# Kernel tuning notes

Measured on AMD Instinct MI355X. Metric: run time of the kernel, lower is better.

## Reference

```python
import jax, jax.numpy as jnp
import numpy as np

EMBED_DIM = 64
HIDDEN_DIM = 320
CONTEXT_DIM = 768

def setup_inputs() -> dict:
    key = jax.random.key(0)
    k1, k2, k3, k4, k5 = jax.random.split(key, 5)
    B, T, S = 4, 4096, 4096
    tokens = jax.random.normal(k1, (B, T, HIDDEN_DIM), dtype=jnp.float32)
    context = jax.random.normal(k2, (B, S, CONTEXT_DIM), dtype=jnp.float32)
    # nn.Linear(in, out, bias=False) weights, stored as [out, in] like torch
    sq = 1.0 / np.sqrt(HIDDEN_DIM)
    sk = 1.0 / np.sqrt(CONTEXT_DIM)
    Wq = jax.random.uniform(k3, (EMBED_DIM, HIDDEN_DIM), minval=-sq, maxval=sq, dtype=jnp.float32)
    Wk = jax.random.uniform(k4, (EMBED_DIM, CONTEXT_DIM), minval=-sk, maxval=sk, dtype=jnp.float32)
    Wv = jax.random.uniform(k5, (HIDDEN_DIM, CONTEXT_DIM), minval=-sk, maxval=sk, dtype=jnp.float32)
    return {"tokens": tokens, "context": context, "Wq": Wq, "Wk": Wk, "Wv": Wv}

def reference(tokens, context, Wq, Wk, Wv):
    # Q: [B,T,E], K: [B,S,E], V: [B,S,Hd]
    Q = jnp.einsum('bth,eh->bte', tokens, Wq)
    K = jnp.einsum('bsc,ec->bse', context, Wk)
    V = jnp.einsum('bsc,hc->bsh', context, Wv)
    scores = jnp.einsum('bte,bse->bts', Q, K) / np.sqrt(EMBED_DIM)
    attn = jax.nn.softmax(scores, axis=-1)  # [B,T,S] full score matrix as in original
    ctx_vecs = jnp.einsum('bts,bsh->bth', attn, V)
    return ctx_vecs
```

## Files before the change

kernel.cpp:

```cpp
#include <hip/hip_runtime.h>
#include <hip/hip_bf16.h>

typedef _Float16 half4_t  __attribute__((ext_vector_type(4)));
typedef _Float16 half8_t  __attribute__((ext_vector_type(8)));
typedef float    float4_t __attribute__((ext_vector_type(4)));

#define MFMA16x32(a, b, c) __builtin_amdgcn_mfma_f32_16x16x32_f16(a, b, c, 0, 0, 0)

template <int KTOT, int NT, int MODE>
__device__ __forceinline__ void proj_body(const float* __restrict__ A,
                                          const float* __restrict__ W,
                                          _Float16* __restrict__ out, float sc,
                                          int m0, int n0, int htg0,
                                          _Float16* Ach, _Float16* Bch) {
  constexpr int NCH = KTOT / 64;
  constexpr int NTIL = NT / 16;
  const int tid = threadIdx.x, w = tid >> 6, lane = tid & 63;
  const int G = lane >> 4, l15 = lane & 15;

  float4_t acc[NTIL];
#pragma unroll
  for (int nt = 0; nt < NTIL; ++nt) acc[nt] = {0.f, 0.f, 0.f, 0.f};

  float4_t areg[4], wreg[NTIL];
  auto ldA = [&](int kc) {
#pragma unroll
    for (int t = 0; t < 4; ++t) {
      int idx = t * 256 + tid;
      areg[t] = *(const float4_t*)(A + (size_t)(m0 + (idx >> 4)) * KTOT + kc * 64 + (idx & 15) * 4);
    }
  };
  auto ldW = [&](int kc) {
#pragma unroll
    for (int t = 0; t < NTIL; ++t) {
      int idx = t * 256 + tid;
      wreg[t] = *(const float4_t*)(W + (size_t)(n0 + (idx >> 4)) * KTOT + kc * 64 + (idx & 15) * 4);
    }
  };

  ldA(0); ldW(0);
  for (int kc = 0; kc < NCH; ++kc) {
    __syncthreads();
#pragma unroll
    for (int t = 0; t < 4; ++t) {
      int idx = t * 256 + tid;
      half4_t h = {(_Float16)areg[t][0], (_Float16)areg[t][1], (_Float16)areg[t][2], (_Float16)areg[t][3]};
      *(half4_t*)(Ach + (idx >> 4) * 72 + (idx & 15) * 4) = h;
    }
#pragma unroll
    for (int t = 0; t < NTIL; ++t) {
      int idx = t * 256 + tid;
      half4_t h = {(_Float16)wreg[t][0], (_Float16)wreg[t][1], (_Float16)wreg[t][2], (_Float16)wreg[t][3]};
      *(half4_t*)(Bch + (idx >> 4) * 72 + (idx & 15) * 4) = h;
    }
    __syncthreads();
    if (kc + 1 < NCH) { ldA(kc + 1); ldW(kc + 1); }
#pragma unroll
    for (int c = 0; c < 2; ++c) {
      half8_t af = *(const half8_t*)(Ach + (w * 16 + l15) * 72 + c * 32 + 8 * G);
#pragma unroll
      for (int nt = 0; nt < NTIL; ++nt) {
        half8_t bf = *(const half8_t*)(Bch + (nt * 16 + l15) * 72 + c * 32 + 8 * G);
        acc[nt] = MFMA16x32(af, bf, acc[nt]);
      }
    }
  }

  if constexpr (MODE <= 1) {
#pragma unroll
    for (int nt = 0; nt < NTIL; ++nt)
#pragma unroll
      for (int r = 0; r < 4; ++r)
        out[(size_t)(m0 + w * 16 + 4 * G + r) * 64 + nt * 16 + l15] = (_Float16)(acc[nt][r] * sc);
  } else {
    __syncthreads();
#pragma unroll
    for (int nt = 0; nt < NTIL; ++nt) {
      half4_t h = {(_Float16)acc[nt][0], (_Float16)acc[nt][1], (_Float16)acc[nt][2], (_Float16)acc[nt][3]};
      *(half4_t*)(Bch + (nt * 16 + l15) * 72 + w * 16 + 4 * G) = h;
    }
    __syncthreads();
#pragma unroll
    for (int rep = 0; rep < 5; ++rep) {
      int idx = w * 5 + rep;
      int c2 = idx / 10, htl = idx % 10;
      half8_t fr = *(const half8_t*)(Bch + (htl * 16 + l15) * 72 + c2 * 32 + 8 * G);
      int sg = m0 + c2 * 32;
      int b = sg >> 12, c2b = (sg & 4095) >> 5;
      int htg = htg0 + htl;
      *(half8_t*)(out + ((size_t)((b * 128 + c2b) * 20 + htg)) * 512 + lane * 8) = fr;
    }
  }
}

__global__ __launch_bounds__(256, 2)
void qkv_proj_kernel(const float* __restrict__ tokens, const float* __restrict__ context,
                     const float* __restrict__ Wq, const float* __restrict__ Wk,
                     const float* __restrict__ Wv, _Float16* __restrict__ Q,
                     _Float16* __restrict__ K, _Float16* __restrict__ V) {
  __shared__ alignas(16) _Float16 smem[16128];
  _Float16* Ach = smem;
  _Float16* Bch = smem + 64 * 72;
  const int bx = blockIdx.x;
  const float qsc = 0.125f * 1.44269504088896f;
  if (bx < 512) {
    int y = bx >> 8, mb = bx & 255;
    proj_body<768, 160, 2>(context, Wv, V, 1.0f, mb * 64, y * 160, y * 10, Ach, Bch);
  } else if (bx < 768) {
    proj_body<768, 64, 1>(context, Wk, K, 1.0f, (bx - 512) * 64, 0, 0, Ach, Bch);
  } else {
    proj_body<320, 64, 0>(tokens, Wq, Q, qsc, (bx - 768) * 64, 0, 0, Ach, Bch);
  }
}

__global__ __launch_bounds__(512, 2)
void flash_kernel(const _Float16* __restrict__ Qg, const _Float16* __restrict__ Kg,
                  const _Float16* __restrict__ Vt, float* __restrict__ out) {
  __shared__ alignas(16) _Float16 kbuf[2][2048];
  __shared__ alignas(16) _Float16 pbuf[2][2048];
  __shared__ float larr[2][4][16];
  __shared__ float linv[64];

  const int tid = threadIdx.x, w = tid >> 6, lane = tid & 63;
  const int G = lane >> 4, l15 = lane & 15;
  const int bx = blockIdx.x;
  const int b = (bx & 7) >> 1;
  const int tblk = ((bx & 1) * 32 + (bx >> 3)) * 64;

  const bool is_pv = (w < 4);
  const int sw = w - 4;
  const int stile = sw & 1, tthalf = sw >> 1;
  const int t2 = tid & 255;
  const int s_loc = t2 >> 3, e8 = t2 & 7;
  const int kdst = ((s_loc >> 4) * 2 + (e8 >> 2)) * 512 + ((e8 & 3) * 16 + (s_loc & 15)) * 8;
  const _Float16* kg = Kg + (size_t)(b * 4096) * 64 + s_loc * 64 + e8 * 8;
  const _Float16* vt_b = Vt + (size_t)b * 1310720;

  half8_t qf[2][2];
  float la[2] = {0.f, 0.f};
  float4_t oa[4][5];
#pragma unroll
  for (int tt = 0; tt < 4; ++tt)
#pragma unroll
    for (int ht = 0; ht < 5; ++ht) oa[tt][ht] = {0.f, 0.f, 0.f, 0.f};
  half8_t vcur[5], vnxt[5];

  if (!is_pv) {
    uint4 k0 = *(const uint4*)(kg);
    uint4 k1 = *(const uint4*)(kg + 2048);
    *(uint4*)(&kbuf[0][kdst]) = k0;
    *(uint4*)(&kbuf[1][kdst]) = k1;
#pragma unroll
    for (int tt2 = 0; tt2 < 2; ++tt2) {
      int tt = tthalf * 2 + tt2;
#pragma unroll
      for (int c = 0; c < 2; ++c)
        qf[tt2][c] = *(const half8_t*)(Qg + (size_t)(b * 4096 + tblk + tt * 16 + l15) * 64 + c * 32 + 8 * G);
    }
  }
  __syncthreads();

  if (is_pv) {
#pragma unroll
    for (int ht = 0; ht < 5; ++ht)
      vcur[ht] = *(const half8_t*)(vt_b + (w * 5 + ht) * 512 + lane * 8);
  } else {
    half8_t af[2];
#pragma unroll
    for (int c = 0; c < 2; ++c)
      af[c] = *(const half8_t*)(&kbuf[0][(stile * 2 + c) * 512 + lane * 8]);
#pragma unroll
    for (int tt2 = 0; tt2 < 2; ++tt2) {
      float4_t sa = {0.f, 0.f, 0.f, 0.f};
#pragma unroll
      for (int c = 0; c < 2; ++c) sa = MFMA16x32(af[c], qf[tt2][c], sa);
      float e0 = exp2f(sa[0]), e1 = exp2f(sa[1]), e2 = exp2f(sa[2]), e3 = exp2f(sa[3]);
      la[tt2] += (e0 + e1) + (e2 + e3);
      int tt = tthalf * 2 + tt2;
      int Gp = stile * 2 + (G >> 1);
      half4_t p = {(_Float16)e0, (_Float16)e1, (_Float16)e2, (_Float16)e3};
      *(half4_t*)(&pbuf[0][tt * 512 + (Gp * 16 + l15) * 8 + 4 * (G & 1)]) = p;
    }
  }
  __syncthreads();

  for (int i = 0; i < 128; ++i) {
    if (is_pv) {
      if (i < 127) {
#pragma unroll
        for (int ht = 0; ht < 5; ++ht)
          vnxt[ht] = *(const half8_t*)(vt_b + (size_t)(i + 1) * 10240 + (w * 5 + ht) * 512 + lane * 8);
      }
      half8_t pa[4];
#pragma unroll
      for (int tt = 0; tt < 4; ++tt)
        pa[tt] = *(const half8_t*)(&pbuf[i & 1][tt * 512 + lane * 8]);
#pragma unroll
      for (int ht = 0; ht < 5; ++ht)
#pragma unroll
        for (int tt = 0; tt < 4; ++tt) oa[tt][ht] = MFMA16x32(pa[tt], vcur[ht], oa[tt][ht]);
#pragma unroll
      for (int ht = 0; ht < 5; ++ht) vcur[ht] = vnxt[ht];
    } else if (i < 127) {
      uint4 kreg;
      if (i < 126) kreg = *(const uint4*)(kg + (size_t)(i + 2) * 2048);
      half8_t af[2];
#pragma unroll
      for (int c = 0; c < 2; ++c)
        af[c] = *(const half8_t*)(&kbuf[(i + 1) & 1][(stile * 2 + c) * 512 + lane * 8]);
#pragma unroll
      for (int tt2 = 0; tt2 < 2; ++tt2) {
        float4_t sa = {0.f, 0.f, 0.f, 0.f};
#pragma unroll
        for (int c = 0; c < 2; ++c) sa = MFMA16x32(af[c], qf[tt2][c], sa);
        float e0 = exp2f(sa[0]), e1 = exp2f(sa[1]), e2 = exp2f(sa[2]), e3 = exp2f(sa[3]);
        la[tt2] += (e0 + e1) + (e2 + e3);
        int tt = tthalf * 2 + tt2;
        int Gp = stile * 2 + (G >> 1);
        half4_t p = {(_Float16)e0, (_Float16)e1, (_Float16)e2, (_Float16)e3};
        *(half4_t*)(&pbuf[(i + 1) & 1][tt * 512 + (Gp * 16 + l15) * 8 + 4 * (G & 1)]) = p;
      }
      if (i < 126) *(uint4*)(&kbuf[i & 1][kdst]) = kreg;
    }
    __syncthreads();
  }

  if (!is_pv) {
#pragma unroll
    for (int tt2 = 0; tt2 < 2; ++tt2) {
      float v = la[tt2];
      v += __shfl_xor(v, 16);
      v += __shfl_xor(v, 32);
      if (lane < 16) larr[stile][tthalf * 2 + tt2][l15] = v;
    }
  }
  __syncthreads();
  if (tid < 64) linv[tid] = 1.0f / (larr[0][tid >> 4][tid & 15] + larr[1][tid >> 4][tid & 15]);
  __syncthreads();
  if (is_pv) {
#pragma unroll
    for (int tt = 0; tt < 4; ++tt)
#pragma unroll
      for (int r = 0; r < 4; ++r) {
        float inv = linv[tt * 16 + 4 * G + r];
        size_t row = (size_t)(b * 4096 + tblk + tt * 16 + 4 * G + r) * 320;
#pragma unroll
        for (int ht = 0; ht < 5; ++ht)
          out[row + w * 80 + ht * 16 + l15] = oa[tt][ht][r] * inv;
      }
  }
}

extern "C" void kernel_launch(void* const* d_in, const int* in_sizes, int n_in,
                              void* d_out, int out_size, void* d_ws, size_t ws_size,
                              hipStream_t stream) {
  const float* tokens  = (const float*)d_in[0];
  const float* context = (const float*)d_in[1];
  const float* Wq      = (const float*)d_in[2];
  const float* Wk      = (const float*)d_in[3];
  const float* Wv      = (const float*)d_in[4];

  _Float16* Qws = (_Float16*)d_ws;
  _Float16* Kws = Qws + (size_t)1048576;
  _Float16* Vws = Kws + (size_t)1048576;

  qkv_proj_kernel<<<dim3(1024), 256, 0, stream>>>(tokens, context, Wq, Wk, Wv,
                                                  Qws, Kws, Vws);
  flash_kernel<<<dim3(256), 512, 0, stream>>>(Qws, Kws, Vws, (float*)d_out);
}
```

Measured before the change: 208.0 us.

## Batch four S-tiles per barrier with 8-deep K/P ring buffers

The producer/consumer flash loop now syncs once per group of four 32-key tiles instead of every tile. K and P shared buffers grow to eight stages so the score warps run four tiles ahead of the PV warps, and the K prefetch loads four tiles per group. The intent is to cut barrier overhead and give the two warp groups slack to run out of step. In exchange, LDS use grows roughly fourfold (about 64KB), which may limit two blocks per CU. Register pressure also rises from the extra K prefetch registers.

```diff
diff --git a/kernel.cpp b/kernel.cpp
--- a/kernel.cpp
+++ b/kernel.cpp
@@ -116,8 +116,8 @@
 __global__ __launch_bounds__(512, 2)
 void flash_kernel(const _Float16* __restrict__ Qg, const _Float16* __restrict__ Kg,
                   const _Float16* __restrict__ Vt, float* __restrict__ out) {
-  __shared__ alignas(16) _Float16 kbuf[2][2048];
-  __shared__ alignas(16) _Float16 pbuf[2][2048];
+  __shared__ alignas(16) _Float16 kbuf[8][2048];
+  __shared__ alignas(16) _Float16 pbuf[8][2048];
   __shared__ float larr[2][4][16];
   __shared__ float linv[64];
 
@@ -128,10 +128,9 @@
   const int tblk = ((bx & 1) * 32 + (bx >> 3)) * 64;
 
   const bool is_pv = (w < 4);
-  const int sw = w - 4;
+  const int sw = w & 3;
   const int stile = sw & 1, tthalf = sw >> 1;
-  const int t2 = tid & 255;
-  const int s_loc = t2 >> 3, e8 = t2 & 7;
+  const int s_loc = sw * 8 + (lane & 7), e8 = lane >> 3;
   const int kdst = ((s_loc >> 4) * 2 + (e8 >> 2)) * 512 + ((e8 & 3) * 16 + (s_loc & 15)) * 8;
   const _Float16* kg = Kg + (size_t)(b * 4096) * 64 + s_loc * 64 + e8 * 8;
   const _Float16* vt_b = Vt + (size_t)b * 1310720;
@@ -143,32 +142,13 @@
   for (int tt = 0; tt < 4; ++tt)
 #pragma unroll
     for (int ht = 0; ht < 5; ++ht) oa[tt][ht] = {0.f, 0.f, 0.f, 0.f};
-  half8_t vcur[5], vnxt[5];
-
-  if (!is_pv) {
-    uint4 k0 = *(const uint4*)(kg);
-    uint4 k1 = *(const uint4*)(kg + 2048);
-    *(uint4*)(&kbuf[0][kdst]) = k0;
-    *(uint4*)(&kbuf[1][kdst]) = k1;
-#pragma unroll
-    for (int tt2 = 0; tt2 < 2; ++tt2) {
-      int tt = tthalf * 2 + tt2;
-#pragma unroll
-      for (int c = 0; c < 2; ++c)
-        qf[tt2][c] = *(const half8_t*)(Qg + (size_t)(b * 4096 + tblk + tt * 16 + l15) * 64 + c * 32 + 8 * G);
-    }
-  }
-  __syncthreads();
-
-  if (is_pv) {
-#pragma unroll
-    for (int ht = 0; ht < 5; ++ht)
-      vcur[ht] = *(const half8_t*)(vt_b + (w * 5 + ht) * 512 + lane * 8);
-  } else {
+  half8_t vb[2][5];
+
+  auto st_step = [&](int j) {
     half8_t af[2];
 #pragma unroll
     for (int c = 0; c < 2; ++c)
-      af[c] = *(const half8_t*)(&kbuf[0][(stile * 2 + c) * 512 + lane * 8]);
+      af[c] = *(const half8_t*)(&kbuf[j & 7][(stile * 2 + c) * 512 + lane * 8]);
 #pragma unroll
     for (int tt2 = 0; tt2 < 2; ++tt2) {
       float4_t sa = {0.f, 0.f, 0.f, 0.f};
@@ -179,50 +159,71 @@
       int tt = tthalf * 2 + tt2;
       int Gp = stile * 2 + (G >> 1);
       half4_t p = {(_Float16)e0, (_Float16)e1, (_Float16)e2, (_Float16)e3};
-      *(half4_t*)(&pbuf[0][tt * 512 + (Gp * 16 + l15) * 8 + 4 * (G & 1)]) = p;
-    }
+      *(half4_t*)(&pbuf[j & 7][tt * 512 + (Gp * 16 + l15) * 8 + 4 * (G & 1)]) = p;
+    }
+  };
+
+  if (!is_pv) {
+#pragma unroll
+    for (int c = 0; c < 8; ++c) {
+      uint4 k = *(const uint4*)(kg + (size_t)c * 2048);
+      *(uint4*)(&kbuf[c][kdst]) = k;
+    }
+#pragma unroll
+    for (int tt2 = 0; tt2 < 2; ++tt2) {
+      int tt = tthalf * 2 + tt2;
+#pragma unroll
+      for (int c = 0; c < 2; ++c)
+        qf[tt2][c] = *(const half8_t*)(Qg + (size_t)(b * 4096 + tblk + tt * 16 + l15) * 64 + c * 32 + 8 * G);
+    }
+  } else {
+#pragma unroll
+    for (int ht = 0; ht < 5; ++ht)
+      vb[0][ht] = *(const half8_t*)(vt_b + (w * 5 + ht) * 512 + lane * 8);
   }
   __syncthreads();
-
-  for (int i = 0; i < 128; ++i) {
+  if (!is_pv) {
+#pragma unroll
+    for (int j = 0; j < 4; ++j) st_step(j);
+  }
+
+  for (int g = 0; g < 32; ++g) {
+    __syncthreads();
+    const int base = g * 4;
     if (is_pv) {
-      if (i < 127) {
+#pragma unroll
+      for (int u = 0; u < 4; ++u) {
+        const int i = base + u;
+        if (i < 127) {
+#pragma unroll
+          for (int ht = 0; ht < 5; ++ht)
+            vb[(u + 1) & 1][ht] = *(const half8_t*)(vt_b + (size_t)(i + 1) * 10240 + (w * 5 + ht) * 512 + lane * 8);
+        }
+        half8_t pa[4];
+#pragma unroll
+        for (int tt = 0; tt < 4; ++tt)
+          pa[tt] = *(const half8_t*)(&pbuf[i & 7][tt * 512 + lane * 8]);
 #pragma unroll
         for (int ht = 0; ht < 5; ++ht)
-          vnxt[ht] = *(const half8_t*)(vt_b + (size_t)(i + 1) * 10240 + (w * 5 + ht) * 512 + lane * 8);
-      }
-      half8_t pa[4];
-#pragma unroll
-      for (int tt = 0; tt < 4; ++tt)
-        pa[tt] = *(const half8_t*)(&pbuf[i & 1][tt * 512 + lane * 8]);
-#pragma unroll
-      for (int ht = 0; ht < 5; ++ht)
-#pragma unroll
-        for (int tt = 0; tt < 4; ++tt) oa[tt][ht] = MFMA16x32(pa[tt], vcur[ht], oa[tt][ht]);
-#pragma unroll
-      for (int ht = 0; ht < 5; ++ht) vcur[ht] = vnxt[ht];
-    } else if (i < 127) {
-      uint4 kreg;
-      if (i < 126) kreg = *(const uint4*)(kg + (size_t)(i + 2) * 2048);
-      half8_t af[2];
-#pragma unroll
-      for (int c = 0; c < 2; ++c)
-        af[c] = *(const half8_t*)(&kbuf[(i + 1) & 1][(stile * 2 + c) * 512 + lane * 8]);
-#pragma unroll
-      for (int tt2 = 0; tt2 < 2; ++tt2) {
-        float4_t sa = {0.f, 0.f, 0.f, 0.f};
-#pragma unroll
-        for (int c = 0; c < 2; ++c) sa = MFMA16x32(af[c], qf[tt2][c], sa);
-        float e0 = exp2f(sa[0]), e1 = exp2f(sa[1]), e2 = exp2f(sa[2]), e3 = exp2f(sa[3]);
-        la[tt2] += (e0 + e1) + (e2 + e3);
-        int tt = tthalf * 2 + tt2;
-        int Gp = stile * 2 + (G >> 1);
-        half4_t p = {(_Float16)e0, (_Float16)e1, (_Float16)e2, (_Float16)e3};
-        *(half4_t*)(&pbuf[(i + 1) & 1][tt * 512 + (Gp * 16 + l15) * 8 + 4 * (G & 1)]) = p;
-      }
-      if (i < 126) *(uint4*)(&kbuf[i & 1][kdst]) = kreg;
-    }
-    __syncthreads();
+#pragma unroll
+          for (int tt = 0; tt < 4; ++tt) oa[tt][ht] = MFMA16x32(pa[tt], vb[u & 1][ht], oa[tt][ht]);
+      }
+    } else {
+      uint4 kr[4];
+      if (base < 120) {
+#pragma unroll
+        for (int u = 0; u < 4; ++u)
+          kr[u] = *(const uint4*)(kg + (size_t)(base + 8 + u) * 2048);
+      }
+#pragma unroll
+      for (int u = 0; u < 4; ++u)
+        if (base + u < 124) st_step(base + u + 4);
+      if (base < 120) {
+#pragma unroll
+        for (int u = 0; u < 4; ++u)
+          *(uint4*)(&kbuf[(base + u) & 7][kdst]) = kr[u];
+      }
+    }
   }
 
   if (!is_pv) {
```

Result: slower. 242.9 us (+16.8%).

## Deepen K prefetch to four LDS stages and unroll main loop by two

Applied to the files above, without the earlier changes.

The K tile ring buffer in shared memory grows from 2 to 4 stages, so each global K load is issued two iterations before it is written to LDS. This gives more latency slack to the score/softmax warps. The main loop is unrolled by two so the V double-buffer registers alternate by index instead of being copied each step. The remapped K-load thread indexing also makes each wave's global load coalesce differently. The cost is more LDS per block and more registers held for in-flight K loads, which could strain occupancy at 2 blocks of 512 threads.

```diff
diff --git a/kernel.cpp b/kernel.cpp
--- a/kernel.cpp
+++ b/kernel.cpp
@@ -116,7 +116,7 @@
 __global__ __launch_bounds__(512, 2)
 void flash_kernel(const _Float16* __restrict__ Qg, const _Float16* __restrict__ Kg,
                   const _Float16* __restrict__ Vt, float* __restrict__ out) {
-  __shared__ alignas(16) _Float16 kbuf[2][2048];
+  __shared__ alignas(16) _Float16 kbuf[4][2048];
   __shared__ alignas(16) _Float16 pbuf[2][2048];
   __shared__ float larr[2][4][16];
   __shared__ float linv[64];
@@ -128,10 +128,9 @@
   const int tblk = ((bx & 1) * 32 + (bx >> 3)) * 64;
 
   const bool is_pv = (w < 4);
-  const int sw = w - 4;
+  const int sw = w & 3;
   const int stile = sw & 1, tthalf = sw >> 1;
-  const int t2 = tid & 255;
-  const int s_loc = t2 >> 3, e8 = t2 & 7;
+  const int s_loc = sw * 8 + (lane & 7), e8 = lane >> 3;
   const int kdst = ((s_loc >> 4) * 2 + (e8 >> 2)) * 512 + ((e8 & 3) * 16 + (s_loc & 15)) * 8;
   const _Float16* kg = Kg + (size_t)(b * 4096) * 64 + s_loc * 64 + e8 * 8;
   const _Float16* vt_b = Vt + (size_t)b * 1310720;
@@ -143,32 +142,14 @@
   for (int tt = 0; tt < 4; ++tt)
 #pragma unroll
     for (int ht = 0; ht < 5; ++ht) oa[tt][ht] = {0.f, 0.f, 0.f, 0.f};
-  half8_t vcur[5], vnxt[5];
-
-  if (!is_pv) {
-    uint4 k0 = *(const uint4*)(kg);
-    uint4 k1 = *(const uint4*)(kg + 2048);
-    *(uint4*)(&kbuf[0][kdst]) = k0;
-    *(uint4*)(&kbuf[1][kdst]) = k1;
-#pragma unroll
-    for (int tt2 = 0; tt2 < 2; ++tt2) {
-      int tt = tthalf * 2 + tt2;
-#pragma unroll
-      for (int c = 0; c < 2; ++c)
-        qf[tt2][c] = *(const half8_t*)(Qg + (size_t)(b * 4096 + tblk + tt * 16 + l15) * 64 + c * 32 + 8 * G);
-    }
-  }
-  __syncthreads();
-
-  if (is_pv) {
-#pragma unroll
-    for (int ht = 0; ht < 5; ++ht)
-      vcur[ht] = *(const half8_t*)(vt_b + (w * 5 + ht) * 512 + lane * 8);
-  } else {
+  half8_t vb[2][5];
+  uint4 kreg[2];
+
+  auto st_step = [&](int j) {
     half8_t af[2];
 #pragma unroll
     for (int c = 0; c < 2; ++c)
-      af[c] = *(const half8_t*)(&kbuf[0][(stile * 2 + c) * 512 + lane * 8]);
+      af[c] = *(const half8_t*)(&kbuf[j & 3][(stile * 2 + c) * 512 + lane * 8]);
 #pragma unroll
     for (int tt2 = 0; tt2 < 2; ++tt2) {
       float4_t sa = {0.f, 0.f, 0.f, 0.f};
@@ -179,50 +160,60 @@
       int tt = tthalf * 2 + tt2;
       int Gp = stile * 2 + (G >> 1);
       half4_t p = {(_Float16)e0, (_Float16)e1, (_Float16)e2, (_Float16)e3};
-      *(half4_t*)(&pbuf[0][tt * 512 + (Gp * 16 + l15) * 8 + 4 * (G & 1)]) = p;
-    }
-  }
-  __syncthreads();
-
-  for (int i = 0; i < 128; ++i) {
-    if (is_pv) {
-      if (i < 127) {
+      *(half4_t*)(&pbuf[j & 1][tt * 512 + (Gp * 16 + l15) * 8 + 4 * (G & 1)]) = p;
+    }
+  };
+
+  if (!is_pv) {
+    uint4 k0 = *(const uint4*)(kg);
+    uint4 k1 = *(const uint4*)(kg + 2048);
+    uint4 k2 = *(const uint4*)(kg + 4096);
+    kreg[1] = *(const uint4*)(kg + 6144);
+    *(uint4*)(&kbuf[0][kdst]) = k0;
+    *(uint4*)(&kbuf[1][kdst]) = k1;
+    *(uint4*)(&kbuf[2][kdst]) = k2;
+#pragma unroll
+    for (int tt2 = 0; tt2 < 2; ++tt2) {
+      int tt = tthalf * 2 + tt2;
+#pragma unroll
+      for (int c = 0; c < 2; ++c)
+        qf[tt2][c] = *(const half8_t*)(Qg + (size_t)(b * 4096 + tblk + tt * 16 + l15) * 64 + c * 32 + 8 * G);
+    }
+  } else {
+#pragma unroll
+    for (int ht = 0; ht < 5; ++ht)
+      vb[0][ht] = *(const half8_t*)(vt_b + (w * 5 + ht) * 512 + lane * 8);
+  }
+  __syncthreads();
+
+  if (!is_pv) st_step(0);
+  __syncthreads();
+
+  for (int ii = 0; ii < 128; ii += 2) {
+#pragma unroll
+    for (int u = 0; u < 2; ++u) {
+      const int i = ii + u;
+      if (is_pv) {
+        if (i < 127) {
+#pragma unroll
+          for (int ht = 0; ht < 5; ++ht)
+            vb[u ^ 1][ht] = *(const half8_t*)(vt_b + (size_t)(i + 1) * 10240 + (w * 5 + ht) * 512 + lane * 8);
+        }
+        half8_t pa[4];
+#pragma unroll
+        for (int tt = 0; tt < 4; ++tt)
+          pa[tt] = *(const half8_t*)(&pbuf[i & 1][tt * 512 + lane * 8]);
 #pragma unroll
         for (int ht = 0; ht < 5; ++ht)
-          vnxt[ht] = *(const half8_t*)(vt_b + (size_t)(i + 1) * 10240 + (w * 5 + ht) * 512 + lane * 8);
+#pragma unroll
+          for (int tt = 0; tt < 4; ++tt) oa[tt][ht] = MFMA16x32(pa[tt], vb[u][ht], oa[tt][ht]);
+      } else {
+        if (i < 124) kreg[u] = *(const uint4*)(kg + (size_t)(i + 4) * 2048);
+        if (i < 127) st_step(i + 1);
+        if (i < 125) *(uint4*)(&kbuf[(i + 3) & 3][kdst]) = kreg[u ^ 1];
       }
-      half8_t pa[4];
-#pragma unroll
-      for (int tt = 0; tt < 4; ++tt)
-        pa[tt] = *(const half8_t*)(&pbuf[i & 1][tt * 512 + lane * 8]);
-#pragma unroll
-      for (int ht = 0; ht < 5; ++ht)
-#pragma unroll
-        for (int tt = 0; tt < 4; ++tt) oa[tt][ht] = MFMA16x32(pa[tt], vcur[ht], oa[tt][ht]);
-#pragma unroll
-      for (int ht = 0; ht < 5; ++ht) vcur[ht] = vnxt[ht];
-    } else if (i < 127) {
-      uint4 kreg;
-      if (i < 126) kreg = *(const uint4*)(kg + (size_t)(i + 2) * 2048);
-      half8_t af[2];
-#pragma unroll
-      for (int c = 0; c < 2; ++c)
-        af[c] = *(const half8_t*)(&kbuf[(i + 1) & 1][(stile * 2 + c) * 512 + lane * 8]);
-#pragma unroll
-      for (int tt2 = 0; tt2 < 2; ++tt2) {
-        float4_t sa = {0.f, 0.f, 0.f, 0.f};
-#pragma unroll
-        for (int c = 0; c < 2; ++c) sa = MFMA16x32(af[c], qf[tt2][c], sa);
-        float e0 = exp2f(sa[0]), e1 = exp2f(sa[1]), e2 = exp2f(sa[2]), e3 = exp2f(sa[3]);
-        la[tt2] += (e0 + e1) + (e2 + e3);
-        int tt = tthalf * 2 + tt2;
-        int Gp = stile * 2 + (G >> 1);
-        half4_t p = {(_Float16)e0, (_Float16)e1, (_Float16)e2, (_Float16)e3};
-        *(half4_t*)(&pbuf[(i + 1) & 1][tt * 512 + (Gp * 16 + l15) * 8 + 4 * (G & 1)]) = p;
-      }
-      if (i < 126) *(uint4*)(&kbuf[i & 1][kdst]) = kreg;
-    }
-    __syncthreads();
+      __syncthreads();
+    }
   }
 
   if (!is_pv) {
```

After: 233.2 us. +12.1%, slower.

## Pre-convert weights to fp16 and fuse K/V projections into one pass over context

Applied to the files above, without the earlier changes.

Adds a small kernel that converts Wq, Wk and Wv to fp16 once per call. The projection kernel now computes K and all 320 V columns in a single block per 64-row context tile, so context is read once instead of three times (two V halves plus K). B fragments are read directly from global/L2 fp16 weights with register double-buffering instead of being staged through LDS. The cost is an extra launch, far more accumulator registers (24 float4 tiles), and many uncoalesced weight-fragment loads that rely on cache hits.

```diff
diff --git a/kernel.cpp b/kernel.cpp
--- a/kernel.cpp
+++ b/kernel.cpp
@@ -7,109 +7,163 @@
 
 #define MFMA16x32(a, b, c) __builtin_amdgcn_mfma_f32_16x16x32_f16(a, b, c, 0, 0, 0)
 
-template <int KTOT, int NT, int MODE>
-__device__ __forceinline__ void proj_body(const float* __restrict__ A,
-                                          const float* __restrict__ W,
-                                          _Float16* __restrict__ out, float sc,
-                                          int m0, int n0, int htg0,
-                                          _Float16* Ach, _Float16* Bch) {
-  constexpr int NCH = KTOT / 64;
-  constexpr int NTIL = NT / 16;
+__global__ __launch_bounds__(256, 4)
+void wcvt_kernel(const float* __restrict__ Wq, const float* __restrict__ Wk,
+                 const float* __restrict__ Wv, _Float16* __restrict__ o) {
+  const int bx = blockIdx.x, t = threadIdx.x;
+  const float* src; _Float16* dst; int base;
+  if (bx < 10)      { src = Wq; dst = o;         base = bx * 2048; }
+  else if (bx < 34) { src = Wk; dst = o + 20480; base = (bx - 10) * 2048; }
+  else              { src = Wv; dst = o + 69632; base = (bx - 34) * 2048; }
+  const int idx = base + t * 8;
+  float4_t a = *(const float4_t*)(src + idx);
+  float4_t b = *(const float4_t*)(src + idx + 4);
+  half8_t h = {(_Float16)a[0], (_Float16)a[1], (_Float16)a[2], (_Float16)a[3],
+               (_Float16)b[0], (_Float16)b[1], (_Float16)b[2], (_Float16)b[3]};
+  *(half8_t*)(dst + idx) = h;
+}
+
+__global__ __launch_bounds__(256, 2)
+void proj2_kernel(const float* __restrict__ tokens, const float* __restrict__ context,
+                  const _Float16* __restrict__ W16, _Float16* __restrict__ Q,
+                  _Float16* __restrict__ K, _Float16* __restrict__ V) {
+  __shared__ alignas(16) _Float16 smem[27648];
+  _Float16* Ach = smem;
+  _Float16* Vb  = smem + 4608;
   const int tid = threadIdx.x, w = tid >> 6, lane = tid & 63;
   const int G = lane >> 4, l15 = lane & 15;
-
-  float4_t acc[NTIL];
-#pragma unroll
-  for (int nt = 0; nt < NTIL; ++nt) acc[nt] = {0.f, 0.f, 0.f, 0.f};
-
-  float4_t areg[4], wreg[NTIL];
-  auto ldA = [&](int kc) {
-#pragma unroll
-    for (int t = 0; t < 4; ++t) {
-      int idx = t * 256 + tid;
-      areg[t] = *(const float4_t*)(A + (size_t)(m0 + (idx >> 4)) * KTOT + kc * 64 + (idx & 15) * 4);
-    }
-  };
-  auto ldW = [&](int kc) {
-#pragma unroll
-    for (int t = 0; t < NTIL; ++t) {
-      int idx = t * 256 + tid;
-      wreg[t] = *(const float4_t*)(W + (size_t)(n0 + (idx >> 4)) * KTOT + kc * 64 + (idx & 15) * 4);
-    }
-  };
-
-  ldA(0); ldW(0);
-  for (int kc = 0; kc < NCH; ++kc) {
+  const int bx = blockIdx.x;
+
+  if (bx < 256) {
+    const int m0 = bx * 64;
+    const _Float16* Wk16 = W16 + 20480;
+    const _Float16* Wv16 = W16 + 69632;
+
+    float4_t acc[24];
+#pragma unroll
+    for (int nt = 0; nt < 24; ++nt) acc[nt] = {0.f, 0.f, 0.f, 0.f};
+
+    float4_t areg[4];
+    auto ldA = [&](int kc) {
+#pragma unroll
+      for (int t = 0; t < 4; ++t) {
+        int idx = t * 256 + tid;
+        areg[t] = *(const float4_t*)(context + (size_t)(m0 + (idx >> 4)) * 768 + kc * 64 + (idx & 15) * 4);
+      }
+    };
+    auto wfrag = [&](int nt, int c, int kc) -> const _Float16* {
+      return (nt < 4 ? Wk16 + (nt * 16 + l15) * 768
+                     : Wv16 + ((nt - 4) * 16 + l15) * 768) + kc * 64 + c * 32 + 8 * G;
+    };
+
+    ldA(0);
+    for (int kc = 0; kc < 12; ++kc) {
+      __syncthreads();
+#pragma unroll
+      for (int t = 0; t < 4; ++t) {
+        int idx = t * 256 + tid;
+        half4_t h = {(_Float16)areg[t][0], (_Float16)areg[t][1], (_Float16)areg[t][2], (_Float16)areg[t][3]};
+        *(half4_t*)(Ach + (idx >> 4) * 72 + (idx & 15) * 4) = h;
+      }
+      __syncthreads();
+      if (kc + 1 < 12) ldA(kc + 1);
+
+      half8_t af0 = *(const half8_t*)(Ach + (w * 16 + l15) * 72 + 8 * G);
+      half8_t af1 = *(const half8_t*)(Ach + (w * 16 + l15) * 72 + 32 + 8 * G);
+
+      half8_t bf[2][4][2];
+#pragma unroll
+      for (int j = 0; j < 4; ++j)
+#pragma unroll
+        for (int c = 0; c < 2; ++c) bf[0][j][c] = *(const half8_t*)wfrag(j, c, kc);
+#pragma unroll
+      for (int g = 0; g < 6; ++g) {
+        if (g + 1 < 6) {
+#pragma unroll
+          for (int j = 0; j < 4; ++j)
+#pragma unroll
+            for (int c = 0; c < 2; ++c)
+              bf[(g + 1) & 1][j][c] = *(const half8_t*)wfrag((g + 1) * 4 + j, c, kc);
+        }
+#pragma unroll
+        for (int j = 0; j < 4; ++j) acc[g * 4 + j] = MFMA16x32(af0, bf[g & 1][j][0], acc[g * 4 + j]);
+#pragma unroll
+        for (int j = 0; j < 4; ++j) acc[g * 4 + j] = MFMA16x32(af1, bf[g & 1][j][1], acc[g * 4 + j]);
+      }
+    }
+
+#pragma unroll
+    for (int nt = 0; nt < 4; ++nt)
+#pragma unroll
+      for (int r = 0; r < 4; ++r)
+        K[(size_t)(m0 + w * 16 + 4 * G + r) * 64 + nt * 16 + l15] = (_Float16)acc[nt][r];
+
     __syncthreads();
 #pragma unroll
-    for (int t = 0; t < 4; ++t) {
-      int idx = t * 256 + tid;
-      half4_t h = {(_Float16)areg[t][0], (_Float16)areg[t][1], (_Float16)areg[t][2], (_Float16)areg[t][3]};
-      *(half4_t*)(Ach + (idx >> 4) * 72 + (idx & 15) * 4) = h;
-    }
-#pragma unroll
-    for (int t = 0; t < NTIL; ++t) {
-      int idx = t * 256 + tid;
-      half4_t h = {(_Float16)wreg[t][0], (_Float16)wreg[t][1], (_Float16)wreg[t][2], (_Float16)wreg[t][3]};
-      *(half4_t*)(Bch + (idx >> 4) * 72 + (idx & 15) * 4) = h;
+    for (int nt = 4; nt < 24; ++nt) {
+      half4_t h = {(_Float16)acc[nt][0], (_Float16)acc[nt][1], (_Float16)acc[nt][2], (_Float16)acc[nt][3]};
+      *(half4_t*)(Vb + ((nt - 4) * 16 + l15) * 72 + w * 16 + 4 * G) = h;
     }
     __syncthreads();
-    if (kc + 1 < NCH) { ldA(kc + 1); ldW(kc + 1); }
-#pragma unroll
-    for (int c = 0; c < 2; ++c) {
-      half8_t af = *(const half8_t*)(Ach + (w * 16 + l15) * 72 + c * 32 + 8 * G);
-#pragma unroll
-      for (int nt = 0; nt < NTIL; ++nt) {
-        half8_t bf = *(const half8_t*)(Bch + (nt * 16 + l15) * 72 + c * 32 + 8 * G);
-        acc[nt] = MFMA16x32(af, bf, acc[nt]);
-      }
-    }
-  }
-
-  if constexpr (MODE <= 1) {
-#pragma unroll
-    for (int nt = 0; nt < NTIL; ++nt)
-#pragma unroll
-      for (int r = 0; r < 4; ++r)
-        out[(size_t)(m0 + w * 16 + 4 * G + r) * 64 + nt * 16 + l15] = (_Float16)(acc[nt][r] * sc);
-  } else {
-    __syncthreads();
-#pragma unroll
-    for (int nt = 0; nt < NTIL; ++nt) {
-      half4_t h = {(_Float16)acc[nt][0], (_Float16)acc[nt][1], (_Float16)acc[nt][2], (_Float16)acc[nt][3]};
-      *(half4_t*)(Bch + (nt * 16 + l15) * 72 + w * 16 + 4 * G) = h;
-    }
-    __syncthreads();
-#pragma unroll
-    for (int rep = 0; rep < 5; ++rep) {
-      int idx = w * 5 + rep;
-      int c2 = idx / 10, htl = idx % 10;
-      half8_t fr = *(const half8_t*)(Bch + (htl * 16 + l15) * 72 + c2 * 32 + 8 * G);
+#pragma unroll
+    for (int rep = 0; rep < 10; ++rep) {
+      int idx = w * 10 + rep;
+      int c2 = idx / 20, htl = idx % 20;
+      half8_t fr = *(const half8_t*)(Vb + (htl * 16 + l15) * 72 + c2 * 32 + 8 * G);
       int sg = m0 + c2 * 32;
       int b = sg >> 12, c2b = (sg & 4095) >> 5;
-      int htg = htg0 + htl;
-      *(half8_t*)(out + ((size_t)((b * 128 + c2b) * 20 + htg)) * 512 + lane * 8) = fr;
-    }
-  }
-}
-
-__global__ __launch_bounds__(256, 2)
-void qkv_proj_kernel(const float* __restrict__ tokens, const float* __restrict__ context,
-                     const float* __restrict__ Wq, const float* __restrict__ Wk,
-                     const float* __restrict__ Wv, _Float16* __restrict__ Q,
-                     _Float16* __restrict__ K, _Float16* __restrict__ V) {
-  __shared__ alignas(16) _Float16 smem[16128];
-  _Float16* Ach = smem;
-  _Float16* Bch = smem + 64 * 72;
-  const int bx = blockIdx.x;
-  const float qsc = 0.125f * 1.44269504088896f;
-  if (bx < 512) {
-    int y = bx >> 8, mb = bx & 255;
-    proj_body<768, 160, 2>(context, Wv, V, 1.0f, mb * 64, y * 160, y * 10, Ach, Bch);
-  } else if (bx < 768) {
-    proj_body<768, 64, 1>(context, Wk, K, 1.0f, (bx - 512) * 64, 0, 0, Ach, Bch);
+      *(half8_t*)(V + ((size_t)((b * 128 + c2b) * 20 + htl)) * 512 + lane * 8) = fr;
+    }
   } else {
-    proj_body<320, 64, 0>(tokens, Wq, Q, qsc, (bx - 768) * 64, 0, 0, Ach, Bch);
+    const int m0 = (bx - 256) * 64;
+    const float qsc = 0.125f * 1.44269504088896f;
+
+    float4_t acc[4];
+#pragma unroll
+    for (int nt = 0; nt < 4; ++nt) acc[nt] = {0.f, 0.f, 0.f, 0.f};
+
+    float4_t areg[4];
+    auto ldA = [&](int kc) {
+#pragma unroll
+      for (int t = 0; t < 4; ++t) {
+        int idx = t * 256 + tid;
+        areg[t] = *(const float4_t*)(tokens + (size_t)(m0 + (idx >> 4)) * 320 + kc * 64 + (idx & 15) * 4);
+      }
+    };
+
+    ldA(0);
+    for (int kc = 0; kc < 5; ++kc) {
+      __syncthreads();
+#pragma unroll
+      for (int t = 0; t < 4; ++t) {
+        int idx = t * 256 + tid;
+        half4_t h = {(_Float16)areg[t][0], (_Float16)areg[t][1], (_Float16)areg[t][2], (_Float16)areg[t][3]};
+        *(half4_t*)(Ach + (idx >> 4) * 72 + (idx & 15) * 4) = h;
+      }
+      __syncthreads();
+      if (kc + 1 < 5) ldA(kc + 1);
+
+      half8_t af[2];
+#pragma unroll
+      for (int c = 0; c < 2; ++c)
+        af[c] = *(const half8_t*)(Ach + (w * 16 + l15) * 72 + c * 32 + 8 * G);
+      half8_t bq[4][2];
+#pragma unroll
+      for (int nt = 0; nt < 4; ++nt)
+#pragma unroll
+        for (int c = 0; c < 2; ++c)
+          bq[nt][c] = *(const half8_t*)(W16 + (nt * 16 + l15) * 320 + kc * 64 + c * 32 + 8 * G);
+#pragma unroll
+      for (int c = 0; c < 2; ++c)
+#pragma unroll
+        for (int nt = 0; nt < 4; ++nt) acc[nt] = MFMA16x32(af[c], bq[nt][c], acc[nt]);
+    }
+
+#pragma unroll
+    for (int nt = 0; nt < 4; ++nt)
+#pragma unroll
+      for (int r = 0; r < 4; ++r)
+        Q[(size_t)(m0 + w * 16 + 4 * G + r) * 64 + nt * 16 + l15] = (_Float16)(acc[nt][r] * qsc);
   }
 }
 
@@ -264,7 +318,13 @@
   _Float16* Kws = Qws + (size_t)1048576;
   _Float16* Vws = Kws + (size_t)1048576;
 
-  qkv_proj_kernel<<<dim3(1024), 256, 0, stream>>>(tokens, context, Wq, Wk, Wv,
-                                                  Qws, Kws, Vws);
+  const size_t W16_BYTES = (size_t)(20480 + 49152 + 245760) * 2;
+  const size_t BASE = (size_t)14 * 1024 * 1024;
+  _Float16* W16 = (ws_size >= BASE + W16_BYTES)
+                      ? (_Float16*)((char*)d_ws + BASE)
+                      : (_Float16*)d_out;
+
+  wcvt_kernel<<<dim3(154), 256, 0, stream>>>(Wq, Wk, Wv, W16);
+  proj2_kernel<<<dim3(512), 256, 0, stream>>>(tokens, context, W16, Qws, Kws, Vws);
   flash_kernel<<<dim3(256), 512, 0, stream>>>(Qws, Kws, Vws, (float*)d_out);
 }
```

New measurement: 279.5 us. 1.34x slower.
